# Optimization experiments

Hardware: AMD Instinct MI355X
Metric: run time of the kernel (lower is better)

The kernel has to match this reference:

```python
import jax, jax.numpy as jnp
import numpy as np
from jax import lax

# Static model/config sizes
B, ANG, C, H, NF, NB = 1, 9, 3, 128, 16, 2


def get_freq_position(n):
    """Anti-diagonal frequency bands of an n x n angular-DCT grid (python/static)."""
    bands = []
    for i in range(n):
        bands.append(([i], [0]))
    for j in range(1, n):
        bands.append(([n - 1], [j]))
    for item in bands:
        while item[0][0] > 0 and item[1][0] < n - 1:
            item[0].insert(0, item[0][0] - 1)
            item[1].insert(0, item[1][0] + 1)
    return bands


def dct_mat(n):
    """Orthonormal DCT-II matrix (row k = k-th basis)."""
    k = jnp.arange(n, dtype=jnp.float32)[:, None]
    i = jnp.arange(n, dtype=jnp.float32)[None, :]
    m = jnp.cos(jnp.pi * (i + 0.5) * k / n) * jnp.sqrt(2.0 / n)
    return m.at[0].multiply(1.0 / np.sqrt(2.0))


def conv3d(x, w, b):
    # x: (N, Cin, D, H, W), w: (Cout, Cin, 3, 3, 3)
    y = lax.conv_general_dilated(x, w, (1, 1, 1), 'SAME',
                                 dimension_numbers=('NCDHW', 'OIDHW', 'NCDHW'))
    return y + b[None, :, None, None, None]


def branch(cut, wi, bi, a, wb, bb):
    """init conv + NB ResBlock3D (PReLU -> Conv3d, residual), plus outer skip."""
    y0 = conv3d(cut, wi, bi)
    y = y0
    for k in range(NB):
        r = jnp.where(y >= 0, y, a[k] * y)  # PReLU (single-parameter)
        y = y + conv3d(r, wb[k], bb[k])
    return y0 + y


def setup_inputs() -> dict:
    key = jax.random.key(0)
    ks = jax.random.split(key, 32)

    def nrm(k, shape, s=0.05):
        return jax.random.normal(k, shape, dtype=jnp.float32) * s

    inp = {"x": jax.random.normal(ks[0], (B, ANG, ANG, C, H, H), dtype=jnp.float32)}
    i = 1
    for n in ("dc", "lo", "mi", "hi"):
        inp[f"w_{n}_i"] = nrm(ks[i], (NF, C, 3, 3, 3)); i += 1
        inp[f"b_{n}_i"] = nrm(ks[i], (NF,)); i += 1
        inp[f"a_{n}"] = jnp.full((NB,), 0.25, dtype=jnp.float32)
        inp[f"w_{n}"] = nrm(ks[i], (NB, NF, NF, 3, 3, 3)); i += 1
        inp[f"b_{n}"] = nrm(ks[i], (NB, NF)); i += 1
    inp["w_last"] = nrm(ks[i], (C, NF))  # 1x1 Conv2d, no bias
    return inp


def reference(x, w_dc_i, b_dc_i, a_dc, w_dc, b_dc,
              w_lo_i, b_lo_i, a_lo, w_lo, b_lo,
              w_mi_i, b_mi_i, a_mi, w_mi, b_mi,
              w_hi_i, b_hi_i, a_hi, w_hi, b_hi, w_last):
    b, u, v, c, h, w = x.shape
    Da = dct_mat(u)  # angular DCT (u == v)
    Ds = dct_mat(h)  # spatial DCT (h == w)

    # SpaAngDCT: spatial 2D DCT then angular 2D DCT
    xf = jnp.einsum('buvchw,Hh,Ww->buvcHW', x, Ds, Ds)
    xf = jnp.einsum('buvchw,Uu,Vv->bUVchw', xf, Da, Da)

    x_rec = jnp.zeros((b, NF, u, v, h, w), dtype=x.dtype)
    for idx, (ui, vi) in enumerate(get_freq_position(u)):
        if idx == 0:
            p = (w_dc_i, b_dc_i, a_dc, w_dc, b_dc)
        elif idx <= 2:
            p = (w_lo_i, b_lo_i, a_lo, w_lo, b_lo)
        elif idx <= u - 1:
            p = (w_mi_i, b_mi_i, a_mi, w_mi, b_mi)
        else:
            p = (w_hi_i, b_hi_i, a_hi, w_hi, b_hi)
        ua, va = jnp.array(ui), jnp.array(vi)
        cut = xf[:, ua, va].transpose(0, 2, 1, 3, 4)  # (b, c, L, h, w)
        out = branch(cut, *p)                          # (b, NF, L, h, w)
        x_rec = x_rec.at[:, :, ua, va].set(out)        # scatter band back

    # 'b c u v h w -> b c (u h) (v w)' then 1x1 conv (NF -> 3)
    xr = x_rec.transpose(0, 1, 2, 4, 3, 5).reshape(b, NF, u * h, v * w)
    xr = jnp.einsum('bnHW,on->boHW', xr, w_last)
    xr = xr.reshape(b, c, u, h, v, w).transpose(0, 2, 4, 1, 3, 5)  # (b,u,v,c,h,w)

    # InverseSpaAngDCT: angular IDCT then spatial IDCT
    xr = jnp.einsum('bUVchw,Uu,Vv->buvchw', xr, Da, Da)
    xr = jnp.einsum('buvcHW,Hh,Ww->buvchw', xr, Ds, Ds)
    return xr + x
```

## Files before the change

kernel.cpp:

```cpp
#include <hip/hip_runtime.h>
#include <hip/hip_bf16.h>
#include <math.h>

typedef __hip_bfloat16 bf16;
typedef __attribute__((ext_vector_type(8))) short short8;
typedef __attribute__((ext_vector_type(4))) float floatx4;
typedef __attribute__((ext_vector_type(4))) unsigned int uint4v;
typedef __attribute__((ext_vector_type(2))) unsigned int uint2v;

#define HW 16384
#define NSLICE 243

__constant__ int c_s_of_p[81] = {
  0, 1,1, 2,2,2, 3,3,3,3, 4,4,4,4,4, 5,5,5,5,5,5, 6,6,6,6,6,6,6,
  7,7,7,7,7,7,7,7, 8,8,8,8,8,8,8,8,8, 9,9,9,9,9,9,9,9,
  10,10,10,10,10,10,10, 11,11,11,11,11,11, 12,12,12,12,12,
  13,13,13,13, 14,14,14, 15,15, 16};
__constant__ int c_l_of_p[81] = {
  0, 0,1, 0,1,2, 0,1,2,3, 0,1,2,3,4, 0,1,2,3,4,5, 0,1,2,3,4,5,6,
  0,1,2,3,4,5,6,7, 0,1,2,3,4,5,6,7,8, 0,1,2,3,4,5,6,7,
  0,1,2,3,4,5,6, 0,1,2,3,4,5, 0,1,2,3,4, 0,1,2,3, 0,1,2, 0,1, 0};
__constant__ int c_L_of_s[17] = {1,2,3,4,5,6,7,8,9,8,7,6,5,4,3,2,1};
__constant__ int c_g_of_s[17] = {0,1,1,2,2,2,2,2,2,3,3,3,3,3,3,3,3};
__constant__ int c_pos_uv[81] = {
  0,1,3,6,10,15,21,28,36,
  2,4,7,11,16,22,29,37,45,
  5,8,12,17,23,30,38,46,53,
  9,13,18,24,31,39,47,54,60,
  14,19,25,32,40,48,55,61,66,
  20,26,33,41,49,56,62,67,71,
  27,34,42,50,57,63,68,72,75,
  35,43,51,58,64,69,73,76,78,
  44,52,59,65,70,74,77,79,80};

struct WPtrs {
  const float* wi[4]; const float* bi[4]; const float* a[4];
  const float* wb[4]; const float* bb[4]; const float* wl;
};

__device__ __forceinline__ unsigned short f2bf(float f) {
  return __bfloat16_as_ushort(__float2bfloat16(f));
}
__device__ __forceinline__ float bf2f(unsigned short u) {
  return __uint_as_float(((unsigned int)u) << 16);
}
__device__ __forceinline__ float bflo(unsigned int w) {
  return __uint_as_float(w << 16);
}
__device__ __forceinline__ float bfhi(unsigned int w) {
  return __uint_as_float(w & 0xffff0000u);
}
__device__ __forceinline__ unsigned int pack2(float a, float b) {
  return (unsigned int)f2bf(a) | ((unsigned int)f2bf(b) << 16);
}
__device__ __forceinline__ float invprelu(float v, float invA) {
  return (v >= 0.f) ? v : v * invA;
}
__device__ __forceinline__ void bfsplit(float v, unsigned short& hi, unsigned short& lo) {
  unsigned int bits = __float_as_uint(v);
  hi = (unsigned short)(bits >> 16);
  lo = f2bf(v - __uint_as_float(bits & 0xffff0000u));
}
__device__ __forceinline__ void gl_lds16(const void* g, void* l) {
  __builtin_amdgcn_global_load_lds(
      (const __attribute__((address_space(1))) unsigned int*)g,
      (__attribute__((address_space(3))) unsigned int*)l, 16, 0, 0);
}
__device__ __forceinline__ int ldsoff(int plane, int col) {
  return plane * 2112 + ((plane & 3) << 5) + (col << 4);
}

__global__ __launch_bounds__(256) void k_init(WPtrs P, float* DaF,
                                              unsigned short* TFhi, unsigned short* TFlo,
                                              unsigned short* TIhi, unsigned short* TIlo,
                                              unsigned short* Wmf,
                                              float* BiF, float* BbF,
                                              float* AF, float* WlF) {
  const double PI = 3.14159265358979323846;
  int t = blockIdx.x * 256 + threadIdx.x;
  if (t < 81) {
    int U = t / 9, u = t % 9;
    double d = cos(PI * (u + 0.5) * U / 9.0) * sqrt(2.0 / 9.0);
    if (U == 0) d *= (1.0 / sqrt(2.0));
    DaF[t] = (float)d;
  }
  if (t < 16384) {
    int jj = t & 7, lane = (t >> 3) & 63, ks = (t >> 9) & 3, tile = t >> 11;
    int row = tile * 16 + (lane & 15);
    int colk = ks * 32 + (lane >> 4) * 8 + jj;
    double vF = cos(PI * (colk + 0.5) * row / 128.0) * sqrt(2.0 / 128.0);
    if (row == 0) vF *= (1.0 / sqrt(2.0));
    double vI = cos(PI * (row + 0.5) * colk / 128.0) * sqrt(2.0 / 128.0);
    if (colk == 0) vI *= (1.0 / sqrt(2.0));
    unsigned short h, l;
    bfsplit((float)vF, h, l); TFhi[t] = h; TFlo[t] = l;
    bfsplit((float)vI, h, l); TIhi[t] = h; TIlo[t] = l;
  }
  if (t < 92160) {
    int s = t / 7680, r = t % 7680;
    int step = r / 512, r2 = r % 512;
    int lane = r2 >> 3, j = r2 & 7;
    int d = step / 5, i = step % 5;
    int q = lane >> 4, m = lane & 15;
    int tl = 2 * i + (q >> 1);
    int cin = (q & 1) * 8 + j;
    float val = 0.f;
    if (tl <= 8) {
      int ky = tl / 3, kx = tl % 3;
      int tap = d * 9 + ky * 3 + kx;
      if (s < 4) {
        if (cin < 3) val = P.wi[s][(m * 3 + cin) * 27 + tap];
      } else {
        int g = (s - 4) >> 1, k = (s - 4) & 1;
        val = P.wb[g][((k * 16 + m) * 16 + cin) * 27 + tap];
      }
    }
    Wmf[t] = f2bf(val);
  }
  if (t < 64)  BiF[t] = P.bi[t / 16][t % 16];
  if (t < 128) BbF[t] = P.bb[t / 32][t % 32];
  if (t < 8)   AF[t]  = P.a[t / 2][t % 2];
  if (t < 48)  WlF[t] = P.wl[t];
}

__global__ __launch_bounds__(256) void k_dct2(const float* __restrict__ X,
                                              const unsigned short* __restrict__ tabhi,
                                              const unsigned short* __restrict__ tablo,
                                              const float* __restrict__ xres,
                                              float* __restrict__ Yf,
                                              unsigned short* __restrict__ Ybf) {
  __shared__ unsigned short sThi[128 * 136];
  __shared__ unsigned short sTlo[128 * 136];
  int s = blockIdx.x;
  int t = threadIdx.x;
  int lane = t & 63, wv = t >> 6;
  int q = lane >> 4, n16 = lane & 15;
  const float* Xs = X + (size_t)s * HW;

  floatx4 acc[2][8];
#pragma unroll
  for (int mt = 0; mt < 2; mt++)
#pragma unroll
    for (int nt = 0; nt < 8; nt++) acc[mt][nt] = (floatx4){0.f, 0.f, 0.f, 0.f};

#pragma unroll
  for (int ks = 0; ks < 4; ks++) {
    short8 ahi[2], alo[2];
#pragma unroll
    for (int mt = 0; mt < 2; mt++) {
      const float* xp = Xs + (wv * 32 + mt * 16 + n16) * 128 + ks * 32 + q * 8;
      float4 a = *(const float4*)xp;
      float4 b = *(const float4*)(xp + 4);
      union { short8 v; unsigned short u[8]; } H, L;
      float xv[8] = {a.x, a.y, a.z, a.w, b.x, b.y, b.z, b.w};
#pragma unroll
      for (int j = 0; j < 8; j++) bfsplit(xv[j], H.u[j], L.u[j]);
      ahi[mt] = H.v; alo[mt] = L.v;
    }
#pragma unroll
    for (int nt = 0; nt < 8; nt++) {
      int e = nt * 2048 + ks * 512 + lane * 8;
      short8 bh = *(const short8*)(tabhi + e);
      short8 bl = *(const short8*)(tablo + e);
#pragma unroll
      for (int mt = 0; mt < 2; mt++) {
        acc[mt][nt] = __builtin_amdgcn_mfma_f32_16x16x32_bf16(ahi[mt], bl, acc[mt][nt], 0, 0, 0);
        acc[mt][nt] = __builtin_amdgcn_mfma_f32_16x16x32_bf16(alo[mt], bh, acc[mt][nt], 0, 0, 0);
        acc[mt][nt] = __builtin_amdgcn_mfma_f32_16x16x32_bf16(ahi[mt], bh, acc[mt][nt], 0, 0, 0);
      }
    }
  }

#pragma unroll
  for (int mt = 0; mt < 2; mt++)
#pragma unroll
    for (int nt = 0; nt < 8; nt++) {
      int col = nt * 16 + n16;
      int rowb = wv * 32 + mt * 16 + q * 4;
#pragma unroll
      for (int rp = 0; rp < 4; rp += 2) {
        unsigned short h0, l0, h1, l1;
        bfsplit(acc[mt][nt][rp], h0, l0);
        bfsplit(acc[mt][nt][rp + 1], h1, l1);
        int widx = (col * 136 + rowb + rp) >> 1;
        ((unsigned int*)sThi)[widx] = (unsigned int)h0 | ((unsigned int)h1 << 16);
        ((unsigned int*)sTlo)[widx] = (unsigned int)l0 | ((unsigned int)l1 << 16);
      }
    }
  __syncthreads();

#pragma unroll
  for (int mt = 0; mt < 2; mt++)
#pragma unroll
    for (int nt = 0; nt < 8; nt++) acc[mt][nt] = (floatx4){0.f, 0.f, 0.f, 0.f};

#pragma unroll
  for (int ks = 0; ks < 4; ks++) {
    short8 ahi[2], alo[2];
#pragma unroll
    for (int mt = 0; mt < 2; mt++) {
      int e = (wv * 2 + mt) * 2048 + ks * 512 + lane * 8;
      ahi[mt] = *(const short8*)(tabhi + e);
      alo[mt] = *(const short8*)(tablo + e);
    }
#pragma unroll
    for (int nt = 0; nt < 8; nt++) {
      int off = (nt * 16 + n16) * 136 + ks * 32 + q * 8;
      short8 bh = *(const short8*)(sThi + off);
      short8 bl = *(const short8*)(sTlo + off);
#pragma unroll
      for (int mt = 0; mt < 2; mt++) {
        acc[mt][nt] = __builtin_amdgcn_mfma_f32_16x16x32_bf16(ahi[mt], bl, acc[mt][nt], 0, 0, 0);
        acc[mt][nt] = __builtin_amdgcn_mfma_f32_16x16x32_bf16(alo[mt], bh, acc[mt][nt], 0, 0, 0);
        acc[mt][nt] = __builtin_amdgcn_mfma_f32_16x16x32_bf16(ahi[mt], bh, acc[mt][nt], 0, 0, 0);
      }
    }
  }

#pragma unroll
  for (int mt = 0; mt < 2; mt++)
#pragma unroll
    for (int nt = 0; nt < 8; nt++) {
      int row0 = wv * 32 + mt * 16 + q * 4;
      int col = nt * 16 + n16;
#pragma unroll
      for (int r = 0; r < 4; r++) {
        size_t oi = (size_t)s * HW + (size_t)(row0 + r) * 128 + col;
        float v = acc[mt][nt][r];
        if (Ybf) {
          Ybf[oi] = f2bf(v);
        } else {
          if (xres) v += xres[oi];
          Yf[oi] = v;
        }
      }
    }
}

__global__ __launch_bounds__(256) void k_angu(const unsigned short* __restrict__ in,
                                              const float* __restrict__ DaF,
                                              unsigned short* __restrict__ out) {
  __shared__ float sDa[81];
  int t = threadIdx.x;
  if (t < 81) sDa[t] = DaF[t];
  __syncthreads();
  int idx = blockIdx.x * 256 + t;
  int hw = idx & (HW - 1);
  int r = idx >> 14;
  int c = r % 3, v = r / 3;
  float f[9];
#pragma unroll
  for (int u = 0; u < 9; u++) f[u] = bf2f(in[(size_t)((u * 9 + v) * 3 + c) * HW + hw]);
#pragma unroll
  for (int U = 0; U < 9; U++) {
    float acc = 0.f;
#pragma unroll
    for (int u = 0; u < 9; u++) acc += sDa[U * 9 + u] * f[u];
    out[(size_t)((U * 9 + v) * 3 + c) * HW + hw] = f2bf(acc);
  }
}

__global__ __launch_bounds__(256) void k_angv(const unsigned short* __restrict__ in,
                                              const float* __restrict__ DaF,
                                              unsigned short* __restrict__ xf2b) {
  __shared__ float sDa[81];
  int t = threadIdx.x;
  if (t < 81) sDa[t] = DaF[t];
  __syncthreads();
  int idx = blockIdx.x * 256 + t;
  int hw = idx & (HW - 1);
  int r = idx >> 14;
  int c = r % 3, U = r / 3;
  float f[9];
#pragma unroll
  for (int v = 0; v < 9; v++) f[v] = bf2f(in[(size_t)((U * 9 + v) * 3 + c) * HW + hw]);
#pragma unroll
  for (int V = 0; V < 9; V++) {
    float acc = 0.f;
#pragma unroll
    for (int v = 0; v < 9; v++) acc += sDa[V * 9 + v] * f[v];
    size_t base = ((size_t)c_pos_uv[U * 9 + V] * HW + hw) * 4;
    xf2b[base + c] = f2bf(acc);
    if (c == 0) xf2b[base + 3] = 0;
  }
}

__global__ __launch_bounds__(256) void k_angvi(const float* __restrict__ xrb,
                                               const float* __restrict__ DaF,
                                               unsigned short* __restrict__ out) {
  __shared__ float sDa[81];
  int t = threadIdx.x;
  if (t < 81) sDa[t] = DaF[t];
  __syncthreads();
  int idx = blockIdx.x * 256 + t;
  int hw = idx & (HW - 1);
  int r = idx >> 14;
  int c = r % 3, U = r / 3;
  float f[9];
#pragma unroll
  for (int V = 0; V < 9; V++)
    f[V] = xrb[((size_t)c_pos_uv[U * 9 + V] * 3 + c) * HW + hw];
#pragma unroll
  for (int v = 0; v < 9; v++) {
    float acc = 0.f;
#pragma unroll
    for (int V = 0; V < 9; V++) acc += sDa[V * 9 + v] * f[V];
    out[(size_t)((U * 9 + v) * 3 + c) * HW + hw] = f2bf(acc);
  }
}

__global__ __launch_bounds__(256) void k_angui(const unsigned short* __restrict__ in,
                                               const float* __restrict__ DaF,
                                               float* __restrict__ out) {
  __shared__ float sDa[81];
  int t = threadIdx.x;
  if (t < 81) sDa[t] = DaF[t];
  __syncthreads();
  int idx = blockIdx.x * 256 + t;
  int hw = idx & (HW - 1);
  int r = idx >> 14;
  int c = r % 3, v = r / 3;
  float f[9];
#pragma unroll
  for (int U = 0; U < 9; U++) f[U] = bf2f(in[(size_t)((U * 9 + v) * 3 + c) * HW + hw]);
#pragma unroll
  for (int u = 0; u < 9; u++) {
    float acc = 0.f;
#pragma unroll
    for (int U = 0; U < 9; U++) acc += sDa[U * 9 + u] * f[U];
    out[(size_t)((u * 9 + v) * 3 + c) * HW + hw] = acc;
  }
}

__global__ __launch_bounds__(256) void k_conv(const unsigned short* __restrict__ src,
                                              const unsigned short* __restrict__ prevAct,
                                              const unsigned short* __restrict__ act0,
                                              const unsigned short* __restrict__ Wmf,
                                              const float* __restrict__ BiF,
                                              const float* __restrict__ BbF,
                                              const float* __restrict__ AF,
                                              const float* __restrict__ WlF,
                                              int sel,
                                              unsigned short* __restrict__ boutAct,
                                              float* __restrict__ xrbOut) {
  __shared__ unsigned short s_lds[38080];
  int p = blockIdx.y;
  int s = c_s_of_p[p], l = c_l_of_p[p];
  int g = c_g_of_s[s], Ls = c_L_of_s[s];
  int row0 = blockIdx.x * 4;
  int t = threadIdx.x;
  int lane = t & 63, wv = t >> 6;
  int q = lane >> 4, n = lane & 15;

  float aNext = (sel < 2) ? AF[g * 2 + sel] : 0.f;
  float invA  = (sel > 0) ? 1.0f / AF[g * 2 + sel - 1] : 0.f;

  {
    uint4v z = (uint4v){0u, 0u, 0u, 0u};
    for (int i = t; i < 72; i += 256) {
      int plane = i >> 1, col = (i & 1) ? 129 : 0;
      *(uint4v*)((char*)s_lds + ldsoff(plane, col)) = z;
    }
    if (sel == 0) {
      for (int i = t; i < 2340; i += 256) {
        int pl = i / 130, col = i % 130;
        int plane = (pl / 6) * 12 + (pl % 6) * 2 + 1;
        *(uint4v*)((char*)s_lds + ldsoff(plane, col)) = z;
      }
    }
    for (int r = 0; r < 6; r++) {
      int grow = row0 - 1 + r;
      if ((unsigned)grow >= 128u) {
        for (int i = t; i < 780; i += 256) {
          int dh = i / 130, col = i % 130;
          int plane = (dh >> 1) * 12 + r * 2 + (dh & 1);
          *(uint4v*)((char*)s_lds + ldsoff(plane, col)) = z;
        }
      }
    }
  }

  int setIdx = (sel == 0) ? g : (4 + g * 2 + (sel - 1));
  const char* WsetBase = (const char*)Wmf + (size_t)setIdx * 15 * 1024;
  short8 af[3][5];
#pragma unroll
  for (int d = 0; d < 3; d++)
#pragma unroll
    for (int i = 0; i < 5; i++)
      af[d][i] = *(const short8*)(WsetBase + ((d * 5 + i) * 64 + lane) * 16);

  if (sel == 0) {
#pragma unroll
    for (int k = 0; k < 9; k++) {
      int cbase = wv * 64 + k * 256;
      int plane6 = cbase >> 7;
      int colb = cbase & 127;
      int d = plane6 / 6, row = plane6 % 6;
      int l2 = l + d - 1, grow = row0 - 1 + row;
      if (l2 >= 0 && l2 < Ls && (unsigned)grow < 128u) {
        int p2 = p + d - 1;
        int col = colb + lane;
        uint2v v2 = *(const uint2v*)(src + ((size_t)p2 * HW + grow * 128 + col) * 4);
        uint4v val; val.x = v2.x; val.y = v2.y; val.z = 0u; val.w = 0u;
        *(uint4v*)((char*)s_lds + ldsoff(d * 12 + row * 2, col + 1)) = val;
      }
    }
  } else {
#pragma unroll
    for (int k = 0; k < 18; k++) {
      int cbase = wv * 64 + k * 256;
      int plane = cbase >> 7;
      int colb = cbase & 127;
      int d = plane / 12, rh = plane % 12, row = rh >> 1, half = rh & 1;
      int l2 = l + d - 1, grow = row0 - 1 + row;
      if (l2 >= 0 && l2 < Ls && (unsigned)grow < 128u) {
        int p2 = p + d - 1;
        const void* gp = (const void*)(src +
            (((size_t)p2 * HW + (size_t)grow * 128 + colb + lane) * 16 + half * 8));
        void* lp = (void*)((char*)s_lds + ldsoff(plane, colb + 1));
        gl_lds16(gp, lp);
      }
    }
  }
  __syncthreads();

  int off2[3][5];
#pragma unroll
  for (int d = 0; d < 3; d++)
#pragma unroll
    for (int i = 0; i < 5; i++) {
      int tl = 2 * i + (q >> 1);
      if (tl > 8) tl = 8;
      int ky = tl / 3, kx = tl % 3;
      off2[d][i] = ldsoff(d * 12 + (wv + ky) * 2 + (q & 1), n + kx);
    }

  floatx4 acc[8];
#pragma unroll
  for (int cg = 0; cg < 8; cg++) acc[cg] = (floatx4){0.f, 0.f, 0.f, 0.f};

#pragma unroll
  for (int d = 0; d < 3; d++) {
    int l2 = l + d - 1;
    if (l2 < 0 || l2 >= Ls) continue;
#pragma unroll
    for (int cg = 0; cg < 8; cg++) {
#pragma unroll
      for (int i = 0; i < 5; i++) {
        short8 b = *(const short8*)((const char*)s_lds + off2[d][i] + cg * 256);
        acc[cg] = __builtin_amdgcn_mfma_f32_16x16x32_bf16(af[d][i], b, acc[cg], 0, 0, 0);
      }
    }
  }

  const float* bp = (sel == 0) ? (BiF + g * 16) : (BbF + g * 32 + (sel - 1) * 16);
  float bz[4];
#pragma unroll
  for (int r = 0; r < 4; r++) bz[r] = bp[q * 4 + r];
  int h = row0 + wv;

  if (sel < 2) {
#pragma unroll
    for (int cg = 0; cg < 8; cg++) {
      size_t pix = (size_t)p * HW + h * 128 + cg * 16 + n;
      float r0 = acc[cg][0] + bz[0], r1 = acc[cg][1] + bz[1];
      float r2 = acc[cg][2] + bz[2], r3 = acc[cg][3] + bz[3];
      if (sel != 0) {
        uint2v pv = *(const uint2v*)(prevAct + pix * 16 + q * 4);
        r0 += invprelu(bflo(pv.x), invA); r1 += invprelu(bfhi(pv.x), invA);
        r2 += invprelu(bflo(pv.y), invA); r3 += invprelu(bfhi(pv.y), invA);
      }
      r0 = fmaxf(r0, 0.f) + aNext * fminf(r0, 0.f);
      r1 = fmaxf(r1, 0.f) + aNext * fminf(r1, 0.f);
      r2 = fmaxf(r2, 0.f) + aNext * fminf(r2, 0.f);
      r3 = fmaxf(r3, 0.f) + aNext * fminf(r3, 0.f);
      uint2v ov; ov.x = pack2(r0, r1); ov.y = pack2(r2, r3);
      *(uint2v*)(boutAct + pix * 16 + q * 4) = ov;
    }
  } else {
    float invA0 = 1.0f / AF[g * 2];
    float wl0[4], wl1[4], wl2[4];
#pragma unroll
    for (int r = 0; r < 4; r++) {
      wl0[r] = WlF[q * 4 + r];
      wl1[r] = WlF[16 + q * 4 + r];
      wl2[r] = WlF[32 + q * 4 + r];
    }
#pragma unroll
    for (int cg = 0; cg < 8; cg++) {
      size_t pix = (size_t)p * HW + h * 128 + cg * 16 + n;
      float r0 = acc[cg][0] + bz[0], r1 = acc[cg][1] + bz[1];
      float r2 = acc[cg][2] + bz[2], r3 = acc[cg][3] + bz[3];
      uint2v pv = *(const uint2v*)(prevAct + pix * 16 + q * 4);
      r0 += invprelu(bflo(pv.x), invA); r1 += invprelu(bfhi(pv.x), invA);
      r2 += invprelu(bflo(pv.y), invA); r3 += invprelu(bfhi(pv.y), invA);
      uint2v p0 = *(const uint2v*)(act0 + pix * 16 + q * 4);
      r0 += invprelu(bflo(p0.x), invA0); r1 += invprelu(bfhi(p0.x), invA0);
      r2 += invprelu(bflo(p0.y), invA0); r3 += invprelu(bfhi(p0.y), invA0);
      float o0 = wl0[0] * r0 + wl0[1] * r1 + wl0[2] * r2 + wl0[3] * r3;
      float o1 = wl1[0] * r0 + wl1[1] * r1 + wl1[2] * r2 + wl1[3] * r3;
      float o2 = wl2[0] * r0 + wl2[1] * r1 + wl2[2] * r2 + wl2[3] * r3;
      o0 += __shfl_xor(o0, 16); o0 += __shfl_xor(o0, 32);
      o1 += __shfl_xor(o1, 16); o1 += __shfl_xor(o1, 32);
      o2 += __shfl_xor(o2, 16); o2 += __shfl_xor(o2, 32);
      if (q == 0) {
        size_t hw = (size_t)h * 128 + cg * 16 + n;
        xrbOut[((size_t)p * 3 + 0) * HW + hw] = o0;
        xrbOut[((size_t)p * 3 + 1) * HW + hw] = o1;
        xrbOut[((size_t)p * 3 + 2) * HW + hw] = o2;
      }
    }
  }
}

extern "C" void kernel_launch(void* const* d_in, const int* in_sizes, int n_in,
                              void* d_out, int out_size, void* d_ws, size_t ws_size,
                              hipStream_t stream) {
  (void)in_sizes; (void)n_in; (void)out_size; (void)ws_size;
  const float* x = (const float*)d_in[0];
  WPtrs P;
  for (int g = 0; g < 4; g++) {
    int b = 1 + g * 5;
    P.wi[g] = (const float*)d_in[b + 0];
    P.bi[g] = (const float*)d_in[b + 1];
    P.a[g]  = (const float*)d_in[b + 2];
    P.wb[g] = (const float*)d_in[b + 3];
    P.bb[g] = (const float*)d_in[b + 4];
  }
  P.wl = (const float*)d_in[21];

  char* base = (char*)d_ws;
  size_t off = 0;
  auto take = [&](size_t bytes) -> char* {
    char* r = base + off;
    off += (bytes + 255) & ~(size_t)255;
    return r;
  };
  float* DaF = (float*)take(81 * 4);
  unsigned short* TFhi = (unsigned short*)take(16384 * 2);
  unsigned short* TFlo = (unsigned short*)take(16384 * 2);
  unsigned short* TIhi = (unsigned short*)take(16384 * 2);
  unsigned short* TIlo = (unsigned short*)take(16384 * 2);
  unsigned short* Wmf = (unsigned short*)take(92160 * 2);
  float* BiF   = (float*)take(256);
  float* BbF   = (float*)take(512);
  float* AF    = (float*)take(32);
  float* WlF   = (float*)take(192);
  float* R1 = (float*)take((size_t)NSLICE * HW * 4);
  unsigned short* B1 = (unsigned short*)take((size_t)NSLICE * HW * 2);
  unsigned short* B2 = (unsigned short*)take((size_t)NSLICE * HW * 2);
  float* R3 = (float*)take((size_t)NSLICE * HW * 4);
  unsigned short* braw0 = (unsigned short*)take((size_t)81 * 16 * HW * 2);
  unsigned short* braw1 = (unsigned short*)take((size_t)81 * 16 * HW * 2);
  unsigned short* xf2b = (unsigned short*)R3;
  float* xrb = R3;

  k_init<<<360, 256, 0, stream>>>(P, DaF, TFhi, TFlo, TIhi, TIlo,
                                  Wmf, BiF, BbF, AF, WlF);
  k_dct2<<<243, 256, 0, stream>>>(x, TFhi, TFlo, nullptr, nullptr, B1);
  k_angu<<<1728, 256, 0, stream>>>(B1, DaF, B2);
  k_angv<<<1728, 256, 0, stream>>>(B2, DaF, xf2b);
  k_conv<<<dim3(32, 81), 256, 0, stream>>>(xf2b, nullptr, nullptr, Wmf,
                                           BiF, BbF, AF, WlF, 0, braw0, nullptr);
  k_conv<<<dim3(32, 81), 256, 0, stream>>>(braw0, braw0, nullptr, Wmf,
                                           BiF, BbF, AF, WlF, 1, braw1, nullptr);
  k_conv<<<dim3(32, 81), 256, 0, stream>>>(braw1, braw1, braw0, Wmf,
                                           BiF, BbF, AF, WlF, 2, nullptr, xrb);
  k_angvi<<<1728, 256, 0, stream>>>(xrb, DaF, B1);
  k_angui<<<1728, 256, 0, stream>>>(B1, DaF, R1);
  k_dct2<<<243, 256, 0, stream>>>(R1, TIhi, TIlo, x, (float*)d_out, nullptr);
}
```

Baseline: 313.5 us.

## Double-buffer depth slices in conv kernel with 512 threads per block

The conv kernel now stages one depth slice at a time into a two-slot LDS buffer and overlaps the load of the next slice with MFMA work on the current one, instead of loading all three slices up front. Threads per block double to 512, and each wave now covers half a row (4 column groups instead of 8), which halves accumulator registers. LDS per block shrinks, which may raise occupancy. The cost is an extra barrier between slices and less work per wave to hide latency.

```diff
diff --git a/kernel.cpp b/kernel.cpp
--- a/kernel.cpp
+++ b/kernel.cpp
@@ -332,7 +332,7 @@
   }
 }
 
-__global__ __launch_bounds__(256) void k_conv(const unsigned short* __restrict__ src,
+__global__ __launch_bounds__(512) void k_conv(const unsigned short* __restrict__ src,
                                               const unsigned short* __restrict__ prevAct,
                                               const unsigned short* __restrict__ act0,
                                               const unsigned short* __restrict__ Wmf,
@@ -343,7 +343,7 @@
                                               int sel,
                                               unsigned short* __restrict__ boutAct,
                                               float* __restrict__ xrbOut) {
-  __shared__ unsigned short s_lds[38080];
+  __shared__ unsigned short s_lds[25400];
   int p = blockIdx.y;
   int s = c_s_of_p[p], l = c_l_of_p[p];
   int g = c_g_of_s[s], Ls = c_L_of_s[s];
@@ -355,26 +355,33 @@
   float aNext = (sel < 2) ? AF[g * 2 + sel] : 0.f;
   float invA  = (sel > 0) ? 1.0f / AF[g * 2 + sel - 1] : 0.f;
 
+  int dlist[3]; int nv = 0;
+#pragma unroll
+  for (int d = 0; d < 3; d++) {
+    int l2 = l + d - 1;
+    if (l2 >= 0 && l2 < Ls) dlist[nv++] = d;
+  }
+
   {
     uint4v z = (uint4v){0u, 0u, 0u, 0u};
-    for (int i = t; i < 72; i += 256) {
-      int plane = i >> 1, col = (i & 1) ? 129 : 0;
-      *(uint4v*)((char*)s_lds + ldsoff(plane, col)) = z;
+    for (int i = t; i < 48; i += 512) {
+      int gp = i >> 1, col = (i & 1) ? 129 : 0;
+      *(uint4v*)((char*)s_lds + ldsoff(gp, col)) = z;
     }
     if (sel == 0) {
-      for (int i = t; i < 2340; i += 256) {
+      for (int i = t; i < 1560; i += 512) {
         int pl = i / 130, col = i % 130;
-        int plane = (pl / 6) * 12 + (pl % 6) * 2 + 1;
-        *(uint4v*)((char*)s_lds + ldsoff(plane, col)) = z;
+        int gp = (pl / 6) * 12 + (pl % 6) * 2 + 1;
+        *(uint4v*)((char*)s_lds + ldsoff(gp, col)) = z;
       }
     }
     for (int r = 0; r < 6; r++) {
       int grow = row0 - 1 + r;
       if ((unsigned)grow >= 128u) {
-        for (int i = t; i < 780; i += 256) {
-          int dh = i / 130, col = i % 130;
-          int plane = (dh >> 1) * 12 + r * 2 + (dh & 1);
-          *(uint4v*)((char*)s_lds + ldsoff(plane, col)) = z;
+        for (int i = t; i < 520; i += 512) {
+          int bh = i / 130, col = i % 130;
+          int gp = (bh >> 1) * 12 + r * 2 + (bh & 1);
+          *(uint4v*)((char*)s_lds + ldsoff(gp, col)) = z;
         }
       }
     }
@@ -389,80 +396,82 @@
     for (int i = 0; i < 5; i++)
       af[d][i] = *(const short8*)(WsetBase + ((d * 5 + i) * 64 + lane) * 16);
 
-  if (sel == 0) {
-#pragma unroll
-    for (int k = 0; k < 9; k++) {
-      int cbase = wv * 64 + k * 256;
-      int plane6 = cbase >> 7;
-      int colb = cbase & 127;
-      int d = plane6 / 6, row = plane6 % 6;
-      int l2 = l + d - 1, grow = row0 - 1 + row;
-      if (l2 >= 0 && l2 < Ls && (unsigned)grow < 128u) {
-        int p2 = p + d - 1;
-        int col = colb + lane;
-        uint2v v2 = *(const uint2v*)(src + ((size_t)p2 * HW + grow * 128 + col) * 4);
-        uint4v val; val.x = v2.x; val.y = v2.y; val.z = 0u; val.w = 0u;
-        *(uint4v*)((char*)s_lds + ldsoff(d * 12 + row * 2, col + 1)) = val;
-      }
-    }
-  } else {
-#pragma unroll
-    for (int k = 0; k < 18; k++) {
-      int cbase = wv * 64 + k * 256;
-      int plane = cbase >> 7;
-      int colb = cbase & 127;
-      int d = plane / 12, rh = plane % 12, row = rh >> 1, half = rh & 1;
-      int l2 = l + d - 1, grow = row0 - 1 + row;
-      if (l2 >= 0 && l2 < Ls && (unsigned)grow < 128u) {
-        int p2 = p + d - 1;
-        const void* gp = (const void*)(src +
-            (((size_t)p2 * HW + (size_t)grow * 128 + colb + lane) * 16 + half * 8));
-        void* lp = (void*)((char*)s_lds + ldsoff(plane, colb + 1));
-        gl_lds16(gp, lp);
-      }
-    }
-  }
+  int scolb = (wv & 1) * 64;
+
+  int rowl = wv >> 1;
+  int cg0 = (wv & 1) * 4;
+  int off2[5];
+#pragma unroll
+  for (int i = 0; i < 5; i++) {
+    int tl = 2 * i + (q >> 1);
+    if (tl > 8) tl = 8;
+    int ky = tl / 3, kx = tl % 3;
+    off2[i] = ldsoff((rowl + ky) * 2 + (q & 1), n + kx) + cg0 * 256;
+  }
+
+  floatx4 acc[4];
+#pragma unroll
+  for (int cg = 0; cg < 4; cg++) acc[cg] = (floatx4){0.f, 0.f, 0.f, 0.f};
+
+  auto stage = [&](int d, int buf) {
+    int p2 = p + d - 1;
+    if (sel == 0) {
+#pragma unroll
+      for (int k = 0; k < 2; k++) {
+        int i = k * 512 + t;
+        if (i < 768) {
+          int row = i >> 7, col = i & 127;
+          int grow = row0 - 1 + row;
+          if ((unsigned)grow < 128u) {
+            uint2v v2 = *(const uint2v*)(src + ((size_t)p2 * HW + grow * 128 + col) * 4);
+            uint4v val; val.x = v2.x; val.y = v2.y; val.z = 0u; val.w = 0u;
+            *(uint4v*)((char*)s_lds + ldsoff(buf * 12 + row * 2, col + 1)) = val;
+          }
+        }
+      }
+    } else {
+#pragma unroll
+      for (int k = 0; k < 3; k++) {
+        int plane = k * 4 + (wv >> 1);
+        int row = plane >> 1, half = plane & 1;
+        int grow = row0 - 1 + row;
+        if ((unsigned)grow < 128u) {
+          const void* gp = (const void*)(src +
+              (((size_t)p2 * HW + (size_t)grow * 128 + scolb + lane) * 16 + half * 8));
+          void* lp = (void*)((char*)s_lds + ldsoff(buf * 12 + plane, scolb + 1));
+          gl_lds16(gp, lp);
+        }
+      }
+    }
+  };
+
+  stage(dlist[0], 0);
   __syncthreads();
-
-  int off2[3][5];
-#pragma unroll
-  for (int d = 0; d < 3; d++)
-#pragma unroll
-    for (int i = 0; i < 5; i++) {
-      int tl = 2 * i + (q >> 1);
-      if (tl > 8) tl = 8;
-      int ky = tl / 3, kx = tl % 3;
-      off2[d][i] = ldsoff(d * 12 + (wv + ky) * 2 + (q & 1), n + kx);
-    }
-
-  floatx4 acc[8];
-#pragma unroll
-  for (int cg = 0; cg < 8; cg++) acc[cg] = (floatx4){0.f, 0.f, 0.f, 0.f};
-
-#pragma unroll
-  for (int d = 0; d < 3; d++) {
-    int l2 = l + d - 1;
-    if (l2 < 0 || l2 >= Ls) continue;
-#pragma unroll
-    for (int cg = 0; cg < 8; cg++) {
-#pragma unroll
-      for (int i = 0; i < 5; i++) {
-        short8 b = *(const short8*)((const char*)s_lds + off2[d][i] + cg * 256);
-        acc[cg] = __builtin_amdgcn_mfma_f32_16x16x32_bf16(af[d][i], b, acc[cg], 0, 0, 0);
-      }
-    }
+  for (int i = 0; i < nv; i++) {
+    if (i + 1 < nv) stage(dlist[i + 1], (i + 1) & 1);
+    int d = dlist[i];
+    const char* bb = (const char*)s_lds + (i & 1) * 25344;
+#pragma unroll
+    for (int cg = 0; cg < 4; cg++) {
+#pragma unroll
+      for (int j = 0; j < 5; j++) {
+        short8 b = *(const short8*)(bb + off2[j] + cg * 256);
+        acc[cg] = __builtin_amdgcn_mfma_f32_16x16x32_bf16(af[d][j], b, acc[cg], 0, 0, 0);
+      }
+    }
+    if (i + 1 < nv) __syncthreads();
   }
 
   const float* bp = (sel == 0) ? (BiF + g * 16) : (BbF + g * 32 + (sel - 1) * 16);
   float bz[4];
 #pragma unroll
   for (int r = 0; r < 4; r++) bz[r] = bp[q * 4 + r];
-  int h = row0 + wv;
+  int h = row0 + rowl;
 
   if (sel < 2) {
 #pragma unroll
-    for (int cg = 0; cg < 8; cg++) {
-      size_t pix = (size_t)p * HW + h * 128 + cg * 16 + n;
+    for (int cg = 0; cg < 4; cg++) {
+      size_t pix = (size_t)p * HW + h * 128 + (cg0 + cg) * 16 + n;
       float r0 = acc[cg][0] + bz[0], r1 = acc[cg][1] + bz[1];
       float r2 = acc[cg][2] + bz[2], r3 = acc[cg][3] + bz[3];
       if (sel != 0) {
@@ -487,8 +496,8 @@
       wl2[r] = WlF[32 + q * 4 + r];
     }
 #pragma unroll
-    for (int cg = 0; cg < 8; cg++) {
-      size_t pix = (size_t)p * HW + h * 128 + cg * 16 + n;
+    for (int cg = 0; cg < 4; cg++) {
+      size_t pix = (size_t)p * HW + h * 128 + (cg0 + cg) * 16 + n;
       float r0 = acc[cg][0] + bz[0], r1 = acc[cg][1] + bz[1];
       float r2 = acc[cg][2] + bz[2], r3 = acc[cg][3] + bz[3];
       uint2v pv = *(const uint2v*)(prevAct + pix * 16 + q * 4);
@@ -504,7 +513,7 @@
       o1 += __shfl_xor(o1, 16); o1 += __shfl_xor(o1, 32);
       o2 += __shfl_xor(o2, 16); o2 += __shfl_xor(o2, 32);
       if (q == 0) {
-        size_t hw = (size_t)h * 128 + cg * 16 + n;
+        size_t hw = (size_t)h * 128 + (cg0 + cg) * 16 + n;
         xrbOut[((size_t)p * 3 + 0) * HW + hw] = o0;
         xrbOut[((size_t)p * 3 + 1) * HW + hw] = o1;
         xrbOut[((size_t)p * 3 + 2) * HW + hw] = o2;
@@ -560,11 +569,11 @@
   k_dct2<<<243, 256, 0, stream>>>(x, TFhi, TFlo, nullptr, nullptr, B1);
   k_angu<<<1728, 256, 0, stream>>>(B1, DaF, B2);
   k_angv<<<1728, 256, 0, stream>>>(B2, DaF, xf2b);
-  k_conv<<<dim3(32, 81), 256, 0, stream>>>(xf2b, nullptr, nullptr, Wmf,
+  k_conv<<<dim3(32, 81), 512, 0, stream>>>(xf2b, nullptr, nullptr, Wmf,
                                            BiF, BbF, AF, WlF, 0, braw0, nullptr);
-  k_conv<<<dim3(32, 81), 256, 0, stream>>>(braw0, braw0, nullptr, Wmf,
+  k_conv<<<dim3(32, 81), 512, 0, stream>>>(braw0, braw0, nullptr, Wmf,
                                            BiF, BbF, AF, WlF, 1, braw1, nullptr);
-  k_conv<<<dim3(32, 81), 256, 0, stream>>>(braw1, braw1, braw0, Wmf,
+  k_conv<<<dim3(32, 81), 512, 0, stream>>>(braw1, braw1, braw0, Wmf,
                                            BiF, BbF, AF, WlF, 2, nullptr, xrb);
   k_angvi<<<1728, 256, 0, stream>>>(xrb, DaF, B1);
   k_angui<<<1728, 256, 0, stream>>>(B1, DaF, R1);
```

Result: slower. 521.5 us (+66.4%).
